# Performance work log

Measured on AMD Instinct MI355X. Metric: run time of the kernel, lower is better.

## Reference

```python
import jax, jax.numpy as jnp
import numpy as np

T, H, E, I = 512, 2048, 8, 4096
W_SCALE = 0.02  # keep activations numerically sane with randn weights


def setup_inputs() -> dict:
    key = jax.random.key(0)
    k_x, k_r, k_w1, k_w3, k_w2 = jax.random.split(key, 5)
    x = jax.random.normal(k_x, (T, H), dtype=jnp.float32)
    router_logits = jax.random.normal(k_r, (T, E), dtype=jnp.float32)
    w1 = jax.random.normal(k_w1, (E, I, H), dtype=jnp.float32) * W_SCALE  # gate proj (silu branch)
    w3 = jax.random.normal(k_w3, (E, I, H), dtype=jnp.float32) * W_SCALE  # up proj
    w2 = jax.random.normal(k_w2, (E, H, I), dtype=jnp.float32) * W_SCALE  # down proj
    return {"x": x, "router_logits": router_logits, "w1": w1, "w3": w3, "w2": w2}


def reference(x, router_logits, w1, w3, w2):
    # Llama4 routing: top-1 expert, router weight = sigmoid(top logit),
    # applied on the INPUT (apply_router_weight_on_input=True).
    top_logit = jnp.max(router_logits, axis=-1)          # [T]
    expert_idx = jnp.argmax(router_logits, axis=-1)      # [T] int
    scale = jax.nn.sigmoid(top_logit)                    # [T]
    xs = x * scale[:, None]                              # [T, H]

    # Grouped SwiGLU experts (dense over E, combined with one-hot select;
    # faithful to fused grouped-GEMM math of FusedMoE).
    gate = jnp.einsum('th,eih->eti', xs, w1)             # [E, T, I]
    up = jnp.einsum('th,eih->eti', xs, w3)               # [E, T, I]
    h = jax.nn.silu(gate) * up                           # [E, T, I]
    y = jnp.einsum('eti,ehi->eth', h, w2)                # [E, T, H]

    onehot = jax.nn.one_hot(expert_idx, E, dtype=x.dtype)  # [T, E]
    out = jnp.einsum('te,eth->th', onehot, y)            # [T, H]
    return out
```

## Files before the change

### kernel.cpp

```cpp
#include <hip/hip_runtime.h>

#define T_TOK 512
#define HDIM 2048
#define NEXP 8
#define IDIM 4096

typedef float f32x4 __attribute__((ext_vector_type(4)));
typedef __bf16 bf16x8 __attribute__((ext_vector_type(8)));
typedef unsigned short ushort8 __attribute__((ext_vector_type(8)));

static __device__ __forceinline__ unsigned short f2bf(float f) {
    unsigned int u = __float_as_uint(f);
    u = (u + 0x7fffu + ((u >> 16) & 1u)) >> 16;
    return (unsigned short)u;
}

static __device__ __forceinline__ bf16x8 cvt8(const f32x4 lo, const f32x4 hi) {
    bf16x8 r;
#pragma unroll
    for (int q = 0; q < 4; ++q) { r[q] = (__bf16)lo[q]; r[q + 4] = (__bf16)hi[q]; }
    return r;
}

static __device__ __forceinline__ void gload_lds16(const void* g, void* l) {
    auto gp = reinterpret_cast<const unsigned int __attribute__((address_space(1)))*>(
        reinterpret_cast<unsigned long long>(g));
    auto lp = reinterpret_cast<unsigned int __attribute__((address_space(3)))*>(
        static_cast<unsigned int>(reinterpret_cast<unsigned long long>(l)));
    __builtin_amdgcn_global_load_lds(gp, lp, 16, 0, 0);
}

__global__ void k_route(const float* __restrict__ logits,
                        int* __restrict__ off, int* __restrict__ tok,
                        float* __restrict__ scale) {
    __shared__ int cnt[NEXP], cur[NEXP];
    const int t = threadIdx.x;
    if (t < NEXP) cnt[t] = 0;
    __syncthreads();
    float m = logits[t * NEXP];
    int a = 0;
#pragma unroll
    for (int j = 1; j < NEXP; ++j) {
        float v = logits[t * NEXP + j];
        if (v > m) { m = v; a = j; }
    }
    scale[t] = 1.f / (1.f + __expf(-m));
    atomicAdd(&cnt[a], 1);
    __syncthreads();
    if (t == 0) {
        int o = 0;
        for (int e = 0; e < NEXP; ++e) { off[e] = o; cur[e] = o; o += cnt[e]; }
        off[NEXP] = o;
    }
    __syncthreads();
    int r = atomicAdd(&cur[a], 1);
    tok[r] = t;
}

__global__ void k_gather(const float* __restrict__ x, const int* __restrict__ tok,
                         const float* __restrict__ scale,
                         unsigned short* __restrict__ xs) {
    const int pos = blockIdx.x;
    const int t = tok[pos];
    const float s = scale[t];
    const int c = threadIdx.x * 8;
    const float4* src = (const float4*)(x + (size_t)t * HDIM + c);
    float4 v0 = src[0], v1 = src[1];
    ushort8 o;
    o[0] = f2bf(v0.x * s); o[1] = f2bf(v0.y * s);
    o[2] = f2bf(v0.z * s); o[3] = f2bf(v0.w * s);
    o[4] = f2bf(v1.x * s); o[5] = f2bf(v1.y * s);
    o[6] = f2bf(v1.z * s); o[7] = f2bf(v1.w * s);
    *(ushort8*)(xs + (size_t)pos * HDIM + c) = o;
}

__global__ void __launch_bounds__(512, 4)
k_moe1(const unsigned short* __restrict__ xs,
       const float* __restrict__ w1,
       const float* __restrict__ w3,
       const int* __restrict__ off,
       unsigned short* __restrict__ hbuf) {
    __shared__ char smem[49152];

    const int tid = threadIdx.x;
    const int w = tid >> 6, l = tid & 63;
    const int wr = w >> 2, wc = w & 3;
    const int e = blockIdx.x & 7;
    const int n0 = (blockIdx.x >> 3) * 64;
    const int ks0 = (blockIdx.x * 13) & 31;
    const int pos_beg = off[e], pos_end = off[e + 1];

    const char* w1b = (const char*)(w1 + (size_t)e * IDIM * HDIM);
    const char* w3b = (const char*)(w3 + (size_t)e * IDIM * HDIM);
    const char* xsb = (const char*)xs;

    const int ia = w * 2;
    const int arow_off = l >> 3;
    const int asw = ((l & 7) ^ (l >> 3)) << 4;
    const int brow_off = l >> 4;

    for (int m0 = pos_beg; m0 < pos_end; m0 += 128) {
        f32x4 accG[4], accU[4];
#pragma unroll
        for (int i = 0; i < 4; ++i) { accG[i] = (f32x4){0,0,0,0}; accU[i] = (f32x4){0,0,0,0}; }

#pragma unroll 1
        for (int it = 0; it < HDIM / 64; ++it) {
            const int ks = (it + ks0) & 31;
            const int k0 = ks * 64;
#pragma unroll
            for (int j = 0; j < 2; ++j) {
                const int i = ia + j;
                int gr = m0 + i * 8 + arow_off; if (gr > T_TOK - 1) gr = T_TOK - 1;
                gload_lds16(xsb + (size_t)gr * (HDIM * 2) + k0 * 2 + asw, smem + i * 1024);
            }
#pragma unroll
            for (int j = 0; j < 2; ++j) {
                const int i = ia + j;
                const int r = i * 4 + brow_off;
                const size_t so = (size_t)(n0 + r) * (HDIM * 4) + k0 * 4 +
                                  (((l & 15) << 4) ^ ((r & 7) << 4));
                gload_lds16(w1b + so, smem + 16384 + i * 1024);
                gload_lds16(w3b + so, smem + 32768 + i * 1024);
            }
            __syncthreads();

#pragma unroll
            for (int kk = 0; kk < 2; ++kk) {
                bf16x8 a[4];
#pragma unroll
                for (int fm = 0; fm < 4; ++fm) {
                    const int row = wr * 64 + fm * 16 + (l & 15);
                    const int kb = (kk * 64 + ((l >> 4) << 4)) ^ ((l & 7) << 4);
                    a[fm] = *(const bf16x8*)(smem + row * 128 + kb);
                }
                const int rB = wc * 16 + (l & 15);
                const int p0 = (kk * 128 + ((l >> 4) << 5)) ^ ((l & 7) << 4);
                const char* pg = smem + 16384 + rB * 256;
                const char* pu = smem + 32768 + rB * 256;
                f32x4 g0 = *(const f32x4*)(pg + p0);
                f32x4 g1 = *(const f32x4*)(pg + (p0 ^ 16));
                f32x4 u0 = *(const f32x4*)(pu + p0);
                f32x4 u1 = *(const f32x4*)(pu + (p0 ^ 16));
                bf16x8 bg = cvt8(g0, g1);
                bf16x8 bu = cvt8(u0, u1);
#pragma unroll
                for (int fm = 0; fm < 4; ++fm) {
                    accG[fm] = __builtin_amdgcn_mfma_f32_16x16x32_bf16(
                        a[fm], bg, accG[fm], 0, 0, 0);
                    accU[fm] = __builtin_amdgcn_mfma_f32_16x16x32_bf16(
                        a[fm], bu, accU[fm], 0, 0, 0);
                }
            }
            __syncthreads();
        }

#pragma unroll
        for (int fm = 0; fm < 4; ++fm)
#pragma unroll
            for (int r = 0; r < 4; ++r) {
                const int pos = m0 + wr * 64 + fm * 16 + (l >> 4) * 4 + r;
                if (pos < pos_end) {
                    const float gv = accG[fm][r];
                    const float uv = accU[fm][r];
                    const float hv = gv / (1.f + __expf(-gv)) * uv;
                    hbuf[(size_t)pos * IDIM + n0 + wc * 16 + (l & 15)] = f2bf(hv);
                }
            }
    }
}

__global__ void __launch_bounds__(256, 4)
k_moe2(const unsigned short* __restrict__ hbuf,
       const float* __restrict__ w2,
       const int* __restrict__ off,
       const int* __restrict__ tok,
       float* __restrict__ out) {
    __shared__ char smem[20480];

    const int tid = threadIdx.x;
    const int w = tid >> 6, l = tid & 63;
    const int e = blockIdx.x & 7;
    const int n0 = (blockIdx.x >> 3) * 16;
    const int ks0 = (blockIdx.x * 13) & 63;
    const int pos_beg = off[e], pos_end = off[e + 1];
    const char* w2b = (const char*)(w2 + (size_t)e * HDIM * IDIM);
    const char* hb  = (const char*)hbuf;

    const int ia = w * 4;
    const int arow_off = l >> 3;
    const int asw = ((l & 7) ^ (l >> 3)) << 4;
    const int brow_off = l >> 4;

    for (int m0 = pos_beg; m0 < pos_end; m0 += 128) {
        f32x4 acc[2];
        acc[0] = (f32x4){0,0,0,0}; acc[1] = (f32x4){0,0,0,0};

#pragma unroll 1
        for (int it = 0; it < IDIM / 64; ++it) {
            const int ks = (it + ks0) & 63;
            const int k0 = ks * 64;
#pragma unroll
            for (int j = 0; j < 4; ++j) {
                const int i = ia + j;
                int gr = m0 + i * 8 + arow_off; if (gr > T_TOK - 1) gr = T_TOK - 1;
                gload_lds16(hb + (size_t)gr * (IDIM * 2) + k0 * 2 + asw, smem + i * 1024);
            }
            {
                const int r = w * 4 + brow_off;
                const size_t so = (size_t)(n0 + r) * (IDIM * 4) + k0 * 4 +
                                  (((l & 15) << 4) ^ ((r & 7) << 4));
                gload_lds16(w2b + so, smem + 16384 + w * 1024);
            }
            __syncthreads();

#pragma unroll
            for (int kk = 0; kk < 2; ++kk) {
                const int rB = l & 15;
                const int p0 = (kk * 128 + ((l >> 4) << 5)) ^ ((l & 7) << 4);
                const char* pb = smem + 16384 + rB * 256;
                f32x4 b0 = *(const f32x4*)(pb + p0);
                f32x4 b1 = *(const f32x4*)(pb + (p0 ^ 16));
                bf16x8 bb = cvt8(b0, b1);
#pragma unroll
                for (int fm = 0; fm < 2; ++fm) {
                    const int row = w * 32 + fm * 16 + (l & 15);
                    const int kb = (kk * 64 + ((l >> 4) << 4)) ^ ((l & 7) << 4);
                    bf16x8 a = *(const bf16x8*)(smem + row * 128 + kb);
                    acc[fm] = __builtin_amdgcn_mfma_f32_16x16x32_bf16(a, bb, acc[fm], 0, 0, 0);
                }
            }
            __syncthreads();
        }

#pragma unroll
        for (int fm = 0; fm < 2; ++fm)
#pragma unroll
            for (int r = 0; r < 4; ++r) {
                const int pos = m0 + w * 32 + fm * 16 + (l >> 4) * 4 + r;
                if (pos < pos_end) {
                    const int t = tok[pos];
                    out[(size_t)t * HDIM + n0 + (l & 15)] = acc[fm][r];
                }
            }
    }
}

extern "C" void kernel_launch(void* const* d_in, const int* in_sizes, int n_in,
                              void* d_out, int out_size, void* d_ws, size_t ws_size,
                              hipStream_t stream) {
    const float* x      = (const float*)d_in[0];
    const float* logits = (const float*)d_in[1];
    const float* w1     = (const float*)d_in[2];
    const float* w3     = (const float*)d_in[3];
    const float* w2     = (const float*)d_in[4];
    float* out = (float*)d_out;

    char* ws = (char*)d_ws;
    int* off   = (int*)ws;
    int* tok   = (int*)(ws + 64);
    float* scl = (float*)(ws + 64 + 2048);
    unsigned short* xs   = (unsigned short*)(ws + 8192);
    unsigned short* hbuf = (unsigned short*)(ws + 8192 + (size_t)T_TOK * HDIM * 2);

    k_route<<<1, T_TOK, 0, stream>>>(logits, off, tok, scl);
    k_gather<<<T_TOK, 256, 0, stream>>>(x, tok, scl, xs);
    k_moe1<<<NEXP * (IDIM / 64), 512, 0, stream>>>(xs, w1, w3, off, hbuf);
    k_moe2<<<NEXP * (HDIM / 16), 256, 0, stream>>>(hbuf, w2, off, tok, out);
}
```

Baseline: 199.5 us.

## Register-prefetch next K tile in moe1 and widen moe2 N tile to 32

In the gate/up kernel, the direct global-to-LDS loads are replaced by loading the next K slice into registers (weights via nontemporal loads) while the current slice is computed, then storing those registers to LDS. The aim is to hide global latency behind the MFMA work. The down-projection kernel now covers 32 output columns per block with a 2x2 warp arrangement, so each hbuf tile staged in LDS is reused across twice as many columns and only half as many blocks are launched. The costs are extra VGPR pressure from the staged registers, and fewer, larger blocks in moe2, which lowers parallelism.

```diff
diff --git a/kernel.cpp b/kernel.cpp
--- a/kernel.cpp
+++ b/kernel.cpp
@@ -8,6 +8,7 @@
 typedef float f32x4 __attribute__((ext_vector_type(4)));
 typedef __bf16 bf16x8 __attribute__((ext_vector_type(8)));
 typedef unsigned short ushort8 __attribute__((ext_vector_type(8)));
+typedef unsigned int u32x4 __attribute__((ext_vector_type(4)));
 
 static __device__ __forceinline__ unsigned short f2bf(float f) {
     unsigned int u = __float_as_uint(f);
@@ -20,6 +21,10 @@
 #pragma unroll
     for (int q = 0; q < 4; ++q) { r[q] = (__bf16)lo[q]; r[q + 4] = (__bf16)hi[q]; }
     return r;
+}
+
+static __device__ __forceinline__ u32x4 ntload16(const void* p) {
+    return __builtin_nontemporal_load((const u32x4*)p);
 }
 
 static __device__ __forceinline__ void gload_lds16(const void* g, void* l) {
@@ -94,36 +99,51 @@
     const char* w3b = (const char*)(w3 + (size_t)e * IDIM * HDIM);
     const char* xsb = (const char*)xs;
 
-    const int ia = w * 2;
-    const int arow_off = l >> 3;
+    const int i0 = w * 2, i1 = i0 + 1;
     const int asw = ((l & 7) ^ (l >> 3)) << 4;
-    const int brow_off = l >> 4;
+    const int r0 = i0 * 4 + (l >> 4), r1 = i1 * 4 + (l >> 4);
+
+    const char* pw1_0 = w1b + (size_t)(n0 + r0) * (HDIM * 4) + (((l & 15) << 4) ^ ((r0 & 7) << 4));
+    const char* pw1_1 = w1b + (size_t)(n0 + r1) * (HDIM * 4) + (((l & 15) << 4) ^ ((r1 & 7) << 4));
+    const char* pw3_0 = w3b + (size_t)(n0 + r0) * (HDIM * 4) + (((l & 15) << 4) ^ ((r0 & 7) << 4));
+    const char* pw3_1 = w3b + (size_t)(n0 + r1) * (HDIM * 4) + (((l & 15) << 4) ^ ((r1 & 7) << 4));
+
+    u32x4* dA0  = (u32x4*)(smem + i0 * 1024 + (l << 4));
+    u32x4* dA1  = (u32x4*)(smem + i1 * 1024 + (l << 4));
+    u32x4* dB10 = (u32x4*)(smem + 16384 + i0 * 1024 + (l << 4));
+    u32x4* dB11 = (u32x4*)(smem + 16384 + i1 * 1024 + (l << 4));
+    u32x4* dB30 = (u32x4*)(smem + 32768 + i0 * 1024 + (l << 4));
+    u32x4* dB31 = (u32x4*)(smem + 32768 + i1 * 1024 + (l << 4));
 
     for (int m0 = pos_beg; m0 < pos_end; m0 += 128) {
+        int gr0 = m0 + i0 * 8 + (l >> 3); if (gr0 > T_TOK - 1) gr0 = T_TOK - 1;
+        int gr1 = m0 + i1 * 8 + (l >> 3); if (gr1 > T_TOK - 1) gr1 = T_TOK - 1;
+        const char* pa0 = xsb + (size_t)gr0 * (HDIM * 2) + asw;
+        const char* pa1 = xsb + (size_t)gr1 * (HDIM * 2) + asw;
+
         f32x4 accG[4], accU[4];
 #pragma unroll
         for (int i = 0; i < 4; ++i) { accG[i] = (f32x4){0,0,0,0}; accU[i] = (f32x4){0,0,0,0}; }
 
+        u32x4 va0, va1, vb10, vb11, vb30, vb31;
+#define LDREGS(IT)                                                           \
+        {                                                                    \
+            const int kq = (((IT) + ks0) & 31) * 64;                         \
+            va0  = *(const u32x4*)(pa0 + kq * 2);                            \
+            va1  = *(const u32x4*)(pa1 + kq * 2);                            \
+            vb10 = ntload16(pw1_0 + kq * 4);                                 \
+            vb11 = ntload16(pw1_1 + kq * 4);                                 \
+            vb30 = ntload16(pw3_0 + kq * 4);                                 \
+            vb31 = ntload16(pw3_1 + kq * 4);                                 \
+        }
+
+        LDREGS(0)
 #pragma unroll 1
-        for (int it = 0; it < HDIM / 64; ++it) {
-            const int ks = (it + ks0) & 31;
-            const int k0 = ks * 64;
-#pragma unroll
-            for (int j = 0; j < 2; ++j) {
-                const int i = ia + j;
-                int gr = m0 + i * 8 + arow_off; if (gr > T_TOK - 1) gr = T_TOK - 1;
-                gload_lds16(xsb + (size_t)gr * (HDIM * 2) + k0 * 2 + asw, smem + i * 1024);
-            }
-#pragma unroll
-            for (int j = 0; j < 2; ++j) {
-                const int i = ia + j;
-                const int r = i * 4 + brow_off;
-                const size_t so = (size_t)(n0 + r) * (HDIM * 4) + k0 * 4 +
-                                  (((l & 15) << 4) ^ ((r & 7) << 4));
-                gload_lds16(w1b + so, smem + 16384 + i * 1024);
-                gload_lds16(w3b + so, smem + 32768 + i * 1024);
-            }
+        for (int it = 0; it < 32; ++it) {
+            *dA0 = va0; *dA1 = va1;
+            *dB10 = vb10; *dB11 = vb11; *dB30 = vb30; *dB31 = vb31;
             __syncthreads();
+            if (it + 1 < 32) LDREGS(it + 1)
 
 #pragma unroll
             for (int kk = 0; kk < 2; ++kk) {
@@ -154,6 +174,7 @@
             }
             __syncthreads();
         }
+#undef LDREGS
 
 #pragma unroll
         for (int fm = 0; fm < 4; ++fm)
@@ -176,25 +197,28 @@
        const int* __restrict__ off,
        const int* __restrict__ tok,
        float* __restrict__ out) {
-    __shared__ char smem[20480];
+    __shared__ char smem[24576];
 
     const int tid = threadIdx.x;
     const int w = tid >> 6, l = tid & 63;
+    const int wr = w >> 1, wc = w & 1;
     const int e = blockIdx.x & 7;
-    const int n0 = (blockIdx.x >> 3) * 16;
+    const int n0 = (blockIdx.x >> 3) * 32;
     const int ks0 = (blockIdx.x * 13) & 63;
     const int pos_beg = off[e], pos_end = off[e + 1];
     const char* w2b = (const char*)(w2 + (size_t)e * HDIM * IDIM);
     const char* hb  = (const char*)hbuf;
 
     const int ia = w * 4;
+    const int ib = w * 2;
     const int arow_off = l >> 3;
     const int asw = ((l & 7) ^ (l >> 3)) << 4;
     const int brow_off = l >> 4;
 
     for (int m0 = pos_beg; m0 < pos_end; m0 += 128) {
-        f32x4 acc[2];
-        acc[0] = (f32x4){0,0,0,0}; acc[1] = (f32x4){0,0,0,0};
+        f32x4 acc[4];
+#pragma unroll
+        for (int i = 0; i < 4; ++i) acc[i] = (f32x4){0, 0, 0, 0};
 
 #pragma unroll 1
         for (int it = 0; it < IDIM / 64; ++it) {
@@ -206,41 +230,47 @@
                 int gr = m0 + i * 8 + arow_off; if (gr > T_TOK - 1) gr = T_TOK - 1;
                 gload_lds16(hb + (size_t)gr * (IDIM * 2) + k0 * 2 + asw, smem + i * 1024);
             }
-            {
-                const int r = w * 4 + brow_off;
+#pragma unroll
+            for (int j = 0; j < 2; ++j) {
+                const int i = ib + j;
+                const int r = i * 4 + brow_off;
                 const size_t so = (size_t)(n0 + r) * (IDIM * 4) + k0 * 4 +
                                   (((l & 15) << 4) ^ ((r & 7) << 4));
-                gload_lds16(w2b + so, smem + 16384 + w * 1024);
+                gload_lds16(w2b + so, smem + 16384 + i * 1024);
             }
             __syncthreads();
 
 #pragma unroll
             for (int kk = 0; kk < 2; ++kk) {
-                const int rB = l & 15;
+                bf16x8 a[4];
+#pragma unroll
+                for (int fm = 0; fm < 4; ++fm) {
+                    const int row = wr * 64 + fm * 16 + (l & 15);
+                    const int kb = (kk * 64 + ((l >> 4) << 4)) ^ ((l & 7) << 4);
+                    a[fm] = *(const bf16x8*)(smem + row * 128 + kb);
+                }
+                const int rB = wc * 16 + (l & 15);
                 const int p0 = (kk * 128 + ((l >> 4) << 5)) ^ ((l & 7) << 4);
                 const char* pb = smem + 16384 + rB * 256;
                 f32x4 b0 = *(const f32x4*)(pb + p0);
                 f32x4 b1 = *(const f32x4*)(pb + (p0 ^ 16));
                 bf16x8 bb = cvt8(b0, b1);
 #pragma unroll
-                for (int fm = 0; fm < 2; ++fm) {
-                    const int row = w * 32 + fm * 16 + (l & 15);
-                    const int kb = (kk * 64 + ((l >> 4) << 4)) ^ ((l & 7) << 4);
-                    bf16x8 a = *(const bf16x8*)(smem + row * 128 + kb);
-                    acc[fm] = __builtin_amdgcn_mfma_f32_16x16x32_bf16(a, bb, acc[fm], 0, 0, 0);
-                }
+                for (int fm = 0; fm < 4; ++fm)
+                    acc[fm] = __builtin_amdgcn_mfma_f32_16x16x32_bf16(
+                        a[fm], bb, acc[fm], 0, 0, 0);
             }
             __syncthreads();
         }
 
 #pragma unroll
-        for (int fm = 0; fm < 2; ++fm)
+        for (int fm = 0; fm < 4; ++fm)
 #pragma unroll
             for (int r = 0; r < 4; ++r) {
-                const int pos = m0 + w * 32 + fm * 16 + (l >> 4) * 4 + r;
+                const int pos = m0 + wr * 64 + fm * 16 + (l >> 4) * 4 + r;
                 if (pos < pos_end) {
                     const int t = tok[pos];
-                    out[(size_t)t * HDIM + n0 + (l & 15)] = acc[fm][r];
+                    out[(size_t)t * HDIM + n0 + wc * 16 + (l & 15)] = acc[fm][r];
                 }
             }
     }
@@ -266,5 +296,5 @@
     k_route<<<1, T_TOK, 0, stream>>>(logits, off, tok, scl);
     k_gather<<<T_TOK, 256, 0, stream>>>(x, tok, scl, xs);
     k_moe1<<<NEXP * (IDIM / 64), 512, 0, stream>>>(xs, w1, w3, off, hbuf);
-    k_moe2<<<NEXP * (HDIM / 16), 256, 0, stream>>>(hbuf, w2, off, tok, out);
-}
+    k_moe2<<<NEXP * (HDIM / 32), 256, 0, stream>>>(hbuf, w2, off, tok, out);
+}
```

After: 176.1 us. -11.7%, faster.
